# Kernel tuning notes

Hardware: AMD Instinct MI355X
Metric: run time of the kernel (lower is better)

## Reference

```python
import jax, jax.numpy as jnp
import numpy as np

B, N, K, M, CIN, O, OUT = 4, 1024, 30, 8, 9, 64, 512
BN_SCALE = 1.0 / np.sqrt(1.0 + 1e-5)  # eval-mode BatchNorm with default stats/affine


def setup_inputs() -> dict:
    key = jax.random.key(0)
    ks = jax.random.split(key, 8)
    x = jax.random.normal(ks[0], (B, CIN, N), jnp.float32)
    norm_plt = jax.random.normal(ks[1], (B, 3, N), jnp.float32)
    cls_label = jnp.zeros((B, 16), jnp.float32)
    conv1_w = jax.random.normal(ks[2], (64, 18), jnp.float32) * np.sqrt(2.0 / 18.0)
    conv1_b = jnp.zeros((64,), jnp.float32)
    sn_hw = jax.random.normal(ks[3], (4, 16, 28), jnp.float32) * np.sqrt(2.0 / 28.0)
    sn_ow = jax.random.normal(ks[4], (4, M, 16), jnp.float32) * np.sqrt(2.0 / 16.0)
    sn_ob = jnp.zeros((4, M), jnp.float32)
    mats = jax.random.normal(ks[5], (4, 2 * O, M * O), jnp.float32) * np.sqrt(2.0 / (2.0 * O))
    convt_w = jax.random.normal(ks[6], (OUT, 5 * O), jnp.float32) * np.sqrt(2.0 / (5.0 * O))
    return dict(x=x, norm_plt=norm_plt, cls_label=cls_label, conv1_w=conv1_w,
                conv1_b=conv1_b, sn_hw=sn_hw, sn_ow=sn_ow, sn_ob=sn_ob,
                mats=mats, convt_w=convt_w)


def _gather(feat, idx):
    # feat (B,N,C), idx (B,N,K) int -> (B,N,K,C): neighbor feature gather
    return jax.vmap(lambda f, i: f[i])(feat, idx)


def _bn(t):
    return t * BN_SCALE


def reference(x, norm_plt, cls_label, conv1_w, conv1_b, sn_hw, sn_ow, sn_ob, mats, convt_w):
    xt = jnp.transpose(x, (0, 2, 1))                       # (B,N,9)
    sq = jnp.sum(xt * xt, axis=-1)
    neg_d = 2.0 * jnp.einsum('bic,bjc->bij', xt, xt) - sq[:, :, None] - sq[:, None, :]
    _, idx = jax.lax.top_k(neg_d, K)                       # (B,N,K) knn indices

    nbr = _gather(xt, idx)                                 # (B,N,K,9)
    ctr = jnp.broadcast_to(xt[:, :, None, :], nbr.shape)   # (B,N,K,9)
    diff = nbr - ctr
    ed = jnp.linalg.norm(diff, axis=-1, keepdims=True)     # (B,N,K,1)
    xyz = jnp.concatenate([diff, nbr, ctr, ed], axis=-1)   # (B,N,K,28) scorenet input

    # get_graph_feature -> conv1 (1x1) -> BN -> relu -> max over k
    gf = jnp.concatenate([diff, ctr], axis=-1)             # (B,N,K,18)
    h = jax.nn.relu(_bn(jnp.einsum('bnkc,oc->bnko', gf, conv1_w) + conv1_b))
    x1 = jnp.max(h, axis=2)                                # (B,N,64)

    feats = [x1]
    f = x1
    for l in range(4):  # PAConv layers 2..5 (sequential, fixed count)
        hid = jax.nn.relu(_bn(jnp.einsum('bnkc,hc->bnkh', xyz, sn_hw[l])))
        score = jax.nn.softmax(jnp.einsum('bnkh,mh->bnkm', hid, sn_ow[l]) + sn_ob[l], axis=-1)
        kern = mats[l]                                     # (128, M*64)
        # feat_trans_dgcnn: neighbor uses full kernel on [f;f], center uses top half
        point = (jnp.concatenate([f, f], axis=-1) @ kern).reshape(B, N, M, O)
        center = (f @ kern[:O]).reshape(B, N, M, O)
        # assemble_dgcnn: sum_k sum_m score * (point[knn] - center)
        gp = _gather(point.reshape(B, N, M * O), idx).reshape(B, N, K, M, O)
        out = jnp.einsum('bnkm,bnkmo->bno', score, gp) - jnp.einsum('bnkm,bnmo->bno', score, center)
        f = jax.nn.relu(_bn(out))
        feats.append(f)

    xx = jnp.concatenate(feats, axis=-1)                   # (B,N,320)
    xc = jax.nn.relu(_bn(jnp.einsum('bnc,oc->bno', xx, convt_w)))
    return jnp.max(xc, axis=1)                             # (B,512) global max pool
```

## Files before the change

kernel.cpp:

```cpp
#include <hip/hip_runtime.h>
#include <hip/hip_bf16.h>

#define B 4
#define N 1024
#define KNN 30
#define MM 8
#define OO 64
#define OUTC 512
#define HID 16
#define FD 320
#define BNS 0.9999950000374997f

typedef float f32x4 __attribute__((ext_vector_type(4)));
typedef short s16x8 __attribute__((ext_vector_type(8)));

#define OFF_XT     0
#define OFF_SQ     36864
#define OFF_IDX    40960
#define OFF_CVT    163840
#define OFF_K2T    245760
#define OFF_FB     376832

__global__ void __launch_bounds__(256) k_prep(const float* __restrict__ x,
                                              const float* __restrict__ convt_w,
                                              const float* __restrict__ mats,
                                              float* __restrict__ xt,
                                              float* __restrict__ sq,
                                              __hip_bfloat16* __restrict__ cvt_bf,
                                              __hip_bfloat16* __restrict__ k2t_bf,
                                              float* __restrict__ out) {
  __shared__ float tile[64][65];
  if (blockIdx.x < 640) {
    int id = blockIdx.x * 256 + threadIdx.x;
    if (id < B * N) {
      int b = id >> 10, n = id & 1023;
      float s = 0.f;
#pragma unroll
      for (int c = 0; c < 9; c++) {
        float v = x[(b * 9 + c) * N + n];
        xt[id * 9 + c] = v;
        s = fmaf(v, v, s);
      }
      sq[id] = s;
    }
    if (id < B * OUTC) out[id] = 0.f;
    if (id < 512 * 320) cvt_bf[id] = __float2bfloat16(convt_w[id]);
  } else {
    int blk = blockIdx.x - 640;
    int l = blk >> 4, part = (blk >> 3) & 1, m = blk & 7;
    int tr = threadIdx.x >> 6;
    int tc = threadIdx.x & 63;
    const float* src = mats + l * 65536 + (part * 64) * 512 + m * 64;
#pragma unroll
    for (int it = 0; it < 16; it++) {
      int c = it * 4 + tr;
      tile[c][tc] = src[c * 512 + tc];
    }
    __syncthreads();
    __hip_bfloat16* dst = k2t_bf + l * 65536 + part * 512 + m * 64;
#pragma unroll
    for (int it = 0; it < 16; it++) {
      int o = it * 4 + tr;
      dst[o * 1024 + tc] = __float2bfloat16(tile[tc][o]);
    }
  }
}

__global__ void __launch_bounds__(256) k_knn(const float* __restrict__ xt,
                                             const float* __restrict__ sq,
                                             int* __restrict__ idx) {
  int r = threadIdx.x >> 6;
  int lane = threadIdx.x & 63;
  int row = blockIdx.x * 4 + r;
  int b = row >> 10;
  __shared__ unsigned int hist[4][256];
  __shared__ unsigned int cntr[4];
  __shared__ unsigned int bp[4];
  __shared__ int bn[4];
  const float* xb = xt + (b << 10) * 9;
  const float* sb = sq + (b << 10);
  float cx[9];
#pragma unroll
  for (int c = 0; c < 9; c++) cx[c] = xt[row * 9 + c];
  float sqn = sq[row];
  unsigned int key[16];
#pragma unroll
  for (int s = 0; s < 16; s++) {
    int j = s * 64 + lane;
    const float* xj = xb + j * 9;
    float dot = 0.f;
#pragma unroll
    for (int c = 0; c < 9; c++) dot = fmaf(cx[c], xj[c], dot);
    float v = 2.0f * dot - sqn - sb[j];
    unsigned int u = __float_as_uint(v);
    key[s] = u ^ ((unsigned int)(((int)u) >> 31) | 0x80000000u);
  }
  if (lane == 0) cntr[r] = 0;
  unsigned int prefix = 0;
  int need = KNN;
  for (int p = 0; p < 4; p++) {
    int shift = 24 - 8 * p;
    for (int i = lane; i < 256; i += 64) hist[r][i] = 0;
    __syncthreads();
    unsigned int himask = (p == 0) ? 0u : (0xFFFFFFFFu << (shift + 8));
#pragma unroll
    for (int s = 0; s < 16; s++) {
      if ((key[s] & himask) == prefix)
        atomicAdd(&hist[r][(key[s] >> shift) & 255], 1u);
    }
    __syncthreads();
    int c0 = hist[r][4 * lane + 0], c1 = hist[r][4 * lane + 1];
    int c2 = hist[r][4 * lane + 2], c3 = hist[r][4 * lane + 3];
    int lsum = c0 + c1 + c2 + c3;
    int sfx = lsum;
#pragma unroll
    for (int ofs = 1; ofs < 64; ofs <<= 1) {
      int t = __shfl_down(sfx, ofs, 64);
      if (lane + ofs < 64) sfx += t;
    }
    int A3 = sfx - lsum;
    int A2 = A3 + c3, A1 = A2 + c2, A0 = A1 + c1;
    if (A0 < need && need <= A0 + c0) { bp[r] = prefix | ((unsigned)(4 * lane + 0) << shift); bn[r] = need - A0; }
    if (A1 < need && need <= A1 + c1) { bp[r] = prefix | ((unsigned)(4 * lane + 1) << shift); bn[r] = need - A1; }
    if (A2 < need && need <= A2 + c2) { bp[r] = prefix | ((unsigned)(4 * lane + 2) << shift); bn[r] = need - A2; }
    if (A3 < need && need <= A3 + c3) { bp[r] = prefix | ((unsigned)(4 * lane + 3) << shift); bn[r] = need - A3; }
    __syncthreads();
    prefix = bp[r];
    need = bn[r];
  }
  unsigned int T = prefix;
  int above_total = KNN - need;
  int* orow = idx + row * KNN;
#pragma unroll
  for (int s = 0; s < 16; s++) {
    if (key[s] > T) {
      unsigned int pslot = atomicAdd(&cntr[r], 1u);
      orow[pslot] = s * 64 + lane;
    }
  }
  int base = 0;
  for (int s = 0; s < 16; s++) {
    unsigned long long m = __ballot(key[s] == T);
    if (key[s] == T) {
      int rk = base + __popcll(m & ((1ull << lane) - 1ull));
      if (rk < need) orow[above_total + rk] = s * 64 + lane;
    }
    base += __popcll(m);
    if (base >= need) break;
  }
}

__global__ void __launch_bounds__(256) k_conv1(const float* __restrict__ xt,
                                               const int* __restrict__ idx,
                                               const float* __restrict__ w,
                                               const float* __restrict__ bias,
                                               __hip_bfloat16* __restrict__ feats_bf) {
  int row0 = blockIdx.x * 4;
  int t = threadIdx.x;
  int b = row0 >> 10;
  __shared__ float ws[64 * 18];
  __shared__ __align__(16) float diff_s[4][KNN][12];
  __shared__ float ctr_s[4][9];
  for (int i = t; i < 64 * 18; i += 256) ws[i] = w[i];
  if (t < 36) { int r = t / 9, c = t - r * 9; ctr_s[r][c] = xt[(row0 + r) * 9 + c]; }
  __syncthreads();
  if (t < 120) {
    int r = t / KNN, k = t - r * KNN;
    int j = idx[(row0 + r) * KNN + k];
    const float* xj = xt + ((b << 10) + j) * 9;
#pragma unroll
    for (int c = 0; c < 9; c++) diff_s[r][k][c] = xj[c] - ctr_s[r][c];
  }
  __syncthreads();
  int wv = t >> 6, lane = t & 63;
  int row = row0 + wv;
  float wd[9];
#pragma unroll
  for (int c = 0; c < 9; c++) wd[c] = ws[lane * 18 + c];
  float cd = 0.f;
#pragma unroll
  for (int c = 0; c < 9; c++) cd = fmaf(ctr_s[wv][c], ws[lane * 18 + 9 + c], cd);
  float best = -3.0e38f;
  for (int k = 0; k < KNN; k++) {
    const float4* dr = (const float4*)diff_s[wv][k];
    float4 d0 = dr[0], d1 = dr[1], d2v = dr[2];
    float dd = 0.f;
    dd = fmaf(d0.x, wd[0], dd); dd = fmaf(d0.y, wd[1], dd);
    dd = fmaf(d0.z, wd[2], dd); dd = fmaf(d0.w, wd[3], dd);
    dd = fmaf(d1.x, wd[4], dd); dd = fmaf(d1.y, wd[5], dd);
    dd = fmaf(d1.z, wd[6], dd); dd = fmaf(d1.w, wd[7], dd);
    dd = fmaf(d2v.x, wd[8], dd);
    best = fmaxf(best, dd);
  }
  float val = (best + cd + bias[lane]) * BNS;
  feats_bf[row * FD + lane] = __float2bfloat16(fmaxf(val, 0.f));
}

__global__ void __launch_bounds__(256) k_layer(const float* __restrict__ xt,
                                               const int* __restrict__ idx,
                                               const float* __restrict__ hw,
                                               const float* __restrict__ ow,
                                               const float* __restrict__ ob,
                                               const __hip_bfloat16* __restrict__ k2t_bf,
                                               __hip_bfloat16* __restrict__ feats_bf,
                                               int l) {
  int row0 = blockIdx.x * 16;
  int t = threadIdx.x;
  int b = row0 >> 10;
  __shared__ float hws[HID * 28];
  __shared__ float ows[MM * HID];
  __shared__ float obs[MM];
  __shared__ int js[16][KNN];
  __shared__ float ctr[16][9];
  __shared__ __align__(16) float sc[16][KNN][8];
  __shared__ float ssum[16][8];
  __shared__ __align__(16) __hip_bfloat16 Hs[16][1040];
  for (int i = t; i < HID * 28; i += 256) hws[i] = hw[l * HID * 28 + i];
  if (t < MM * HID) ows[t] = ow[l * MM * HID + t];
  if (t < MM) obs[t] = ob[l * MM + t];
  if (t < 144) { int r = t / 9, c = t - r * 9; ctr[r][c] = xt[(row0 + r) * 9 + c]; }
  for (int i = t; i < 16 * KNN; i += 256) {
    int r = i / KNN, k = i - r * KNN;
    js[r][k] = (b << 10) + idx[(row0 + r) * KNN + k];
  }
  __syncthreads();
  for (int i = t; i < 16 * KNN; i += 256) {
    int r = i / KNN, k = i - r * KNN;
    const float* xj = xt + js[r][k] * 9;
    float xv[28];
    float d2 = 0.f;
#pragma unroll
    for (int c = 0; c < 9; c++) {
      float nb = xj[c], ct = ctr[r][c], df = nb - ct;
      xv[c] = df; xv[9 + c] = nb; xv[18 + c] = ct;
      d2 = fmaf(df, df, d2);
    }
    xv[27] = sqrtf(d2);
    float hid[HID];
#pragma unroll
    for (int h = 0; h < HID; h++) {
      float a = 0.f;
#pragma unroll
      for (int c = 0; c < 28; c++) a = fmaf(xv[c], hws[h * 28 + c], a);
      hid[h] = fmaxf(a * BNS, 0.f);
    }
    float lg[MM], mx = -3.0e38f;
#pragma unroll
    for (int m = 0; m < MM; m++) {
      float a = obs[m];
#pragma unroll
      for (int h = 0; h < HID; h++) a = fmaf(hid[h], ows[m * HID + h], a);
      lg[m] = a; mx = fmaxf(mx, a);
    }
    float s = 0.f;
#pragma unroll
    for (int m = 0; m < MM; m++) { lg[m] = __expf(lg[m] - mx); s += lg[m]; }
    float inv = 1.0f / s;
#pragma unroll
    for (int m = 0; m < MM; m++) sc[r][k][m] = lg[m] * inv;
  }
  __syncthreads();
  if (t < 128) {
    int r = t >> 3, m = t & 7;
    float a = 0.f;
#pragma unroll
    for (int k = 0; k < KNN; k++) a += sc[r][k][m];
    ssum[r][m] = a;
  }
  __syncthreads();
  int wv = t >> 6, lane = t & 63;
#pragma unroll
  for (int rr = 0; rr < 4; rr++) {
    int r = wv * 4 + rr;
    int row = row0 + r;
    float g[MM] = {};
#pragma unroll
    for (int k = 0; k < KNN; k++) {
      float fv = __bfloat162float(feats_bf[js[r][k] * FD + l * 64 + lane]);
      const float4* s4 = (const float4*)sc[r][k];
      float4 s0 = s4[0], s1 = s4[1];
      g[0] = fmaf(s0.x, fv, g[0]); g[1] = fmaf(s0.y, fv, g[1]);
      g[2] = fmaf(s0.z, fv, g[2]); g[3] = fmaf(s0.w, fv, g[3]);
      g[4] = fmaf(s1.x, fv, g[4]); g[5] = fmaf(s1.y, fv, g[5]);
      g[6] = fmaf(s1.z, fv, g[6]); g[7] = fmaf(s1.w, fv, g[7]);
    }
    float fn = __bfloat162float(feats_bf[row * FD + l * 64 + lane]);
#pragma unroll
    for (int m = 0; m < MM; m++) {
      Hs[r][m * 64 + lane] = __float2bfloat16(g[m] - ssum[r][m] * fn);
      Hs[r][512 + m * 64 + lane] = __float2bfloat16(g[m]);
    }
  }
  __syncthreads();
  int lr = lane & 15, lk8 = (lane >> 4) * 8;
  const short* Ks2 = (const short*)(k2t_bf + l * 65536);
  const short* brow = Ks2 + (wv * 16 + lr) * 1024 + lk8;
  const short* arow = (const short*)&Hs[lr][lk8];
  f32x4 acc = {0.f, 0.f, 0.f, 0.f};
#pragma unroll 8
  for (int kk = 0; kk < 32; kk++) {
    s16x8 a = *(const s16x8*)(arow + kk * 32);
    s16x8 bb = *(const s16x8*)(brow + kk * 32);
    acc = __builtin_amdgcn_mfma_f32_16x16x32_bf16(a, bb, acc, 0, 0, 0);
  }
#pragma unroll
  for (int i = 0; i < 4; i++) {
    int row = row0 + (lane >> 4) * 4 + i;
    feats_bf[row * FD + (l + 1) * 64 + wv * 16 + lr] =
        __float2bfloat16(fmaxf(acc[i] * BNS, 0.f));
  }
}

__global__ void __launch_bounds__(256) k_final(const __hip_bfloat16* __restrict__ feats_bf,
                                               const __hip_bfloat16* __restrict__ cvt_bf,
                                               float* __restrict__ out) {
  int m0 = (blockIdx.x >> 1) * 16;
  int nhalf = (blockIdx.x & 1) * 256;
  int w = threadIdx.x >> 6;
  int lane = threadIdx.x & 63;
  int lr = lane & 15, lk8 = (lane >> 4) * 8;
  int b = m0 >> 10;
  const short* Fs = (const short*)feats_bf;
  const short* Ws = (const short*)cvt_bf;
  const short* arow = Fs + (m0 + lr) * FD + lk8;
  int nbase = nhalf + w * 64;
  const short* brow = Ws + (nbase + lr) * FD + lk8;
  f32x4 acc[4] = {{0.f, 0.f, 0.f, 0.f}, {0.f, 0.f, 0.f, 0.f},
                  {0.f, 0.f, 0.f, 0.f}, {0.f, 0.f, 0.f, 0.f}};
#pragma unroll
  for (int kk = 0; kk < 10; kk++) {
    int k0 = kk * 32;
    s16x8 a = *(const s16x8*)(arow + k0);
#pragma unroll
    for (int tn = 0; tn < 4; tn++) {
      s16x8 bb = *(const s16x8*)(brow + tn * 16 * FD + k0);
      acc[tn] = __builtin_amdgcn_mfma_f32_16x16x32_bf16(a, bb, acc[tn], 0, 0, 0);
    }
  }
#pragma unroll
  for (int tn = 0; tn < 4; tn++) {
    float mx = fmaxf(fmaxf(acc[tn][0], acc[tn][1]), fmaxf(acc[tn][2], acc[tn][3]));
    mx = fmaxf(mx, __shfl_xor(mx, 16, 64));
    mx = fmaxf(mx, __shfl_xor(mx, 32, 64));
    if ((lane >> 4) == 0) {
      float val = fmaxf(mx * BNS, 0.f);
      int o = nbase + tn * 16 + lr;
      atomicMax((unsigned int*)out + b * OUTC + o, __float_as_uint(val));
    }
  }
}

extern "C" void kernel_launch(void* const* d_in, const int* in_sizes, int n_in,
                              void* d_out, int out_size, void* d_ws, size_t ws_size,
                              hipStream_t stream) {
  const float* x       = (const float*)d_in[0];
  const float* conv1_w = (const float*)d_in[3];
  const float* conv1_b = (const float*)d_in[4];
  const float* sn_hw   = (const float*)d_in[5];
  const float* sn_ow   = (const float*)d_in[6];
  const float* sn_ob   = (const float*)d_in[7];
  const float* mats    = (const float*)d_in[8];
  const float* convt_w = (const float*)d_in[9];
  float* out = (float*)d_out;

  float* w = (float*)d_ws;
  float* xt = w + OFF_XT;
  float* sq = w + OFF_SQ;
  int* idx = (int*)(w + OFF_IDX);
  __hip_bfloat16* cvt_bf = (__hip_bfloat16*)(w + OFF_CVT);
  __hip_bfloat16* k2t_bf = (__hip_bfloat16*)(w + OFF_K2T);
  __hip_bfloat16* feats_bf = (__hip_bfloat16*)(w + OFF_FB);

  k_prep<<<704, 256, 0, stream>>>(x, convt_w, mats, xt, sq, cvt_bf, k2t_bf, out);
  k_knn<<<1024, 256, 0, stream>>>(xt, sq, idx);
  k_conv1<<<1024, 256, 0, stream>>>(xt, idx, conv1_w, conv1_b, feats_bf);
  for (int l = 0; l < 4; l++) {
    k_layer<<<256, 256, 0, stream>>>(xt, idx, sn_hw, sn_ow, sn_ob, k2t_bf, feats_bf, l);
  }
  k_final<<<512, 256, 0, stream>>>(feats_bf, cvt_bf, out);
}
```

Measured before the change: 208.0 us.

## Fuse knn with conv1, precompute all scorenet scores, fold final conv into last layer

```diff
diff --git a/kernel.cpp b/kernel.cpp
--- a/kernel.cpp
+++ b/kernel.cpp
@@ -5,7 +5,6 @@
 #define N 1024
 #define KNN 30
 #define MM 8
-#define OO 64
 #define OUTC 512
 #define HID 16
 #define FD 320
@@ -20,6 +19,7 @@
 #define OFF_CVT    163840
 #define OFF_K2T    245760
 #define OFF_FB     376832
+#define OFF_SC     1032192
 
 __global__ void __launch_bounds__(256) k_prep(const float* __restrict__ x,
                                               const float* __restrict__ convt_w,
@@ -66,17 +66,27 @@
   }
 }
 
-__global__ void __launch_bounds__(256) k_knn(const float* __restrict__ xt,
-                                             const float* __restrict__ sq,
-                                             int* __restrict__ idx) {
-  int r = threadIdx.x >> 6;
-  int lane = threadIdx.x & 63;
+__global__ void __launch_bounds__(256) k_knnc1(const float* __restrict__ xt,
+                                               const float* __restrict__ sq,
+                                               const float* __restrict__ w,
+                                               const float* __restrict__ bias,
+                                               int* __restrict__ idx,
+                                               __hip_bfloat16* __restrict__ feats_bf) {
+  int t = threadIdx.x;
+  int r = t >> 6;
+  int lane = t & 63;
   int row = blockIdx.x * 4 + r;
   int b = row >> 10;
   __shared__ unsigned int hist[4][256];
   __shared__ unsigned int cntr[4];
   __shared__ unsigned int bp[4];
   __shared__ int bn[4];
+  __shared__ int js_l[4][KNN];
+  __shared__ float ws[64 * 18];
+  __shared__ __align__(16) float diff_s[4][KNN][12];
+  __shared__ float ctr_s[4][9];
+  for (int i = t; i < 64 * 18; i += 256) ws[i] = w[i];
+  if (t < 36) { int rr = t / 9, c = t - rr * 9; ctr_s[rr][c] = xt[(blockIdx.x * 4 + rr) * 9 + c]; }
   const float* xb = xt + (b << 10) * 9;
   const float* sb = sq + (b << 10);
   float cx[9];
@@ -115,8 +125,8 @@
     int sfx = lsum;
 #pragma unroll
     for (int ofs = 1; ofs < 64; ofs <<= 1) {
-      int t = __shfl_down(sfx, ofs, 64);
-      if (lane + ofs < 64) sfx += t;
+      int tt = __shfl_down(sfx, ofs, 64);
+      if (lane + ofs < 64) sfx += tt;
     }
     int A3 = sfx - lsum;
     int A2 = A3 + c3, A1 = A2 + c2, A0 = A1 + c1;
@@ -136,6 +146,7 @@
     if (key[s] > T) {
       unsigned int pslot = atomicAdd(&cntr[r], 1u);
       orow[pslot] = s * 64 + lane;
+      js_l[r][pslot] = s * 64 + lane;
     }
   }
   int base = 0;
@@ -143,46 +154,32 @@
     unsigned long long m = __ballot(key[s] == T);
     if (key[s] == T) {
       int rk = base + __popcll(m & ((1ull << lane) - 1ull));
-      if (rk < need) orow[above_total + rk] = s * 64 + lane;
+      if (rk < need) {
+        orow[above_total + rk] = s * 64 + lane;
+        js_l[r][above_total + rk] = s * 64 + lane;
+      }
     }
     base += __popcll(m);
     if (base >= need) break;
   }
-}
-
-__global__ void __launch_bounds__(256) k_conv1(const float* __restrict__ xt,
-                                               const int* __restrict__ idx,
-                                               const float* __restrict__ w,
-                                               const float* __restrict__ bias,
-                                               __hip_bfloat16* __restrict__ feats_bf) {
-  int row0 = blockIdx.x * 4;
-  int t = threadIdx.x;
-  int b = row0 >> 10;
-  __shared__ float ws[64 * 18];
-  __shared__ __align__(16) float diff_s[4][KNN][12];
-  __shared__ float ctr_s[4][9];
-  for (int i = t; i < 64 * 18; i += 256) ws[i] = w[i];
-  if (t < 36) { int r = t / 9, c = t - r * 9; ctr_s[r][c] = xt[(row0 + r) * 9 + c]; }
   __syncthreads();
   if (t < 120) {
-    int r = t / KNN, k = t - r * KNN;
-    int j = idx[(row0 + r) * KNN + k];
+    int rr = t / KNN, k = t - rr * KNN;
+    int j = js_l[rr][k];
     const float* xj = xt + ((b << 10) + j) * 9;
 #pragma unroll
-    for (int c = 0; c < 9; c++) diff_s[r][k][c] = xj[c] - ctr_s[r][c];
-  }
-  __syncthreads();
-  int wv = t >> 6, lane = t & 63;
-  int row = row0 + wv;
+    for (int c = 0; c < 9; c++) diff_s[rr][k][c] = xj[c] - ctr_s[rr][c];
+  }
+  __syncthreads();
   float wd[9];
 #pragma unroll
   for (int c = 0; c < 9; c++) wd[c] = ws[lane * 18 + c];
   float cd = 0.f;
 #pragma unroll
-  for (int c = 0; c < 9; c++) cd = fmaf(ctr_s[wv][c], ws[lane * 18 + 9 + c], cd);
+  for (int c = 0; c < 9; c++) cd = fmaf(ctr_s[r][c], ws[lane * 18 + 9 + c], cd);
   float best = -3.0e38f;
   for (int k = 0; k < KNN; k++) {
-    const float4* dr = (const float4*)diff_s[wv][k];
+    const float4* dr = (const float4*)diff_s[r][k];
     float4 d0 = dr[0], d1 = dr[1], d2v = dr[2];
     float dd = 0.f;
     dd = fmaf(d0.x, wd[0], dd); dd = fmaf(d0.y, wd[1], dd);
@@ -196,89 +193,99 @@
   feats_bf[row * FD + lane] = __float2bfloat16(fmaxf(val, 0.f));
 }
 
-__global__ void __launch_bounds__(256) k_layer(const float* __restrict__ xt,
+__global__ void __launch_bounds__(256) k_score(const float* __restrict__ xt,
                                                const int* __restrict__ idx,
                                                const float* __restrict__ hw,
                                                const float* __restrict__ ow,
                                                const float* __restrict__ ob,
-                                               const __hip_bfloat16* __restrict__ k2t_bf,
-                                               __hip_bfloat16* __restrict__ feats_bf,
-                                               int l) {
+                                               float* __restrict__ score) {
+  __shared__ float hws[4 * 448];
+  __shared__ float ows[4 * 128];
+  __shared__ float obs[32];
+  int t = threadIdx.x;
+  for (int i = t; i < 1792; i += 256) hws[i] = hw[i];
+  for (int i = t; i < 512; i += 256) ows[i] = ow[i];
+  if (t < 32) obs[t] = ob[t];
+  __syncthreads();
+  int id = blockIdx.x * 256 + t;
+  int row = id / KNN;
+  int b = row >> 10;
+  int j = idx[id];
+  const float* xc = xt + row * 9;
+  const float* xj = xt + ((b << 10) + j) * 9;
+  float xv[28];
+  float d2 = 0.f;
+#pragma unroll
+  for (int c = 0; c < 9; c++) {
+    float nb = xj[c], ct = xc[c], df = nb - ct;
+    xv[c] = df; xv[9 + c] = nb; xv[18 + c] = ct;
+    d2 = fmaf(df, df, d2);
+  }
+  xv[27] = sqrtf(d2);
+  for (int l = 0; l < 4; l++) {
+    float hid[HID];
+#pragma unroll
+    for (int h = 0; h < HID; h++) {
+      float a = 0.f;
+#pragma unroll
+      for (int c = 0; c < 28; c++) a = fmaf(xv[c], hws[l * 448 + h * 28 + c], a);
+      hid[h] = fmaxf(a * BNS, 0.f);
+    }
+    float lg[MM], mx = -3.0e38f;
+#pragma unroll
+    for (int m = 0; m < MM; m++) {
+      float a = obs[l * 8 + m];
+#pragma unroll
+      for (int h = 0; h < HID; h++) a = fmaf(hid[h], ows[l * 128 + m * 16 + h], a);
+      lg[m] = a; mx = fmaxf(mx, a);
+    }
+    float s = 0.f;
+#pragma unroll
+    for (int m = 0; m < MM; m++) { lg[m] = __expf(lg[m] - mx); s += lg[m]; }
+    float inv = 1.0f / s;
+    float* so = score + l * 983040 + id * 8;
+    *(float4*)so = make_float4(lg[0] * inv, lg[1] * inv, lg[2] * inv, lg[3] * inv);
+    *(float4*)(so + 4) = make_float4(lg[4] * inv, lg[5] * inv, lg[6] * inv, lg[7] * inv);
+  }
+}
+
+__global__ void __launch_bounds__(512) k_layer2(const int* __restrict__ idx,
+                                                const float* __restrict__ score,
+                                                const __hip_bfloat16* __restrict__ k2t_bf,
+                                                __hip_bfloat16* __restrict__ feats_bf,
+                                                const __hip_bfloat16* __restrict__ cvt_bf,
+                                                float* __restrict__ out,
+                                                int l, int last) {
   int row0 = blockIdx.x * 16;
   int t = threadIdx.x;
   int b = row0 >> 10;
-  __shared__ float hws[HID * 28];
-  __shared__ float ows[MM * HID];
-  __shared__ float obs[MM];
   __shared__ int js[16][KNN];
-  __shared__ float ctr[16][9];
-  __shared__ __align__(16) float sc[16][KNN][8];
   __shared__ float ssum[16][8];
   __shared__ __align__(16) __hip_bfloat16 Hs[16][1040];
-  for (int i = t; i < HID * 28; i += 256) hws[i] = hw[l * HID * 28 + i];
-  if (t < MM * HID) ows[t] = ow[l * MM * HID + t];
-  if (t < MM) obs[t] = ob[l * MM + t];
-  if (t < 144) { int r = t / 9, c = t - r * 9; ctr[r][c] = xt[(row0 + r) * 9 + c]; }
-  for (int i = t; i < 16 * KNN; i += 256) {
+  __shared__ __align__(16) __hip_bfloat16 ftile[16][336];
+  const float* sc_l = score + l * 983040;
+  for (int i = t; i < 16 * KNN; i += 512) {
     int r = i / KNN, k = i - r * KNN;
     js[r][k] = (b << 10) + idx[(row0 + r) * KNN + k];
   }
-  __syncthreads();
-  for (int i = t; i < 16 * KNN; i += 256) {
-    int r = i / KNN, k = i - r * KNN;
-    const float* xj = xt + js[r][k] * 9;
-    float xv[28];
-    float d2 = 0.f;
-#pragma unroll
-    for (int c = 0; c < 9; c++) {
-      float nb = xj[c], ct = ctr[r][c], df = nb - ct;
-      xv[c] = df; xv[9 + c] = nb; xv[18 + c] = ct;
-      d2 = fmaf(df, df, d2);
-    }
-    xv[27] = sqrtf(d2);
-    float hid[HID];
-#pragma unroll
-    for (int h = 0; h < HID; h++) {
-      float a = 0.f;
-#pragma unroll
-      for (int c = 0; c < 28; c++) a = fmaf(xv[c], hws[h * 28 + c], a);
-      hid[h] = fmaxf(a * BNS, 0.f);
-    }
-    float lg[MM], mx = -3.0e38f;
-#pragma unroll
-    for (int m = 0; m < MM; m++) {
-      float a = obs[m];
-#pragma unroll
-      for (int h = 0; h < HID; h++) a = fmaf(hid[h], ows[m * HID + h], a);
-      lg[m] = a; mx = fmaxf(mx, a);
-    }
-    float s = 0.f;
-#pragma unroll
-    for (int m = 0; m < MM; m++) { lg[m] = __expf(lg[m] - mx); s += lg[m]; }
-    float inv = 1.0f / s;
-#pragma unroll
-    for (int m = 0; m < MM; m++) sc[r][k][m] = lg[m] * inv;
-  }
-  __syncthreads();
   if (t < 128) {
     int r = t >> 3, m = t & 7;
     float a = 0.f;
-#pragma unroll
-    for (int k = 0; k < KNN; k++) a += sc[r][k][m];
+    for (int k = 0; k < KNN; k++) a += sc_l[(row0 + r) * 240 + k * 8 + m];
     ssum[r][m] = a;
   }
   __syncthreads();
   int wv = t >> 6, lane = t & 63;
 #pragma unroll
-  for (int rr = 0; rr < 4; rr++) {
-    int r = wv * 4 + rr;
+  for (int rr = 0; rr < 2; rr++) {
+    int r = wv * 2 + rr;
     int row = row0 + r;
+    const float4* srow = (const float4*)(sc_l + row * 240);
     float g[MM] = {};
 #pragma unroll
     for (int k = 0; k < KNN; k++) {
       float fv = __bfloat162float(feats_bf[js[r][k] * FD + l * 64 + lane]);
-      const float4* s4 = (const float4*)sc[r][k];
-      float4 s0 = s4[0], s1 = s4[1];
+      float4 s0 = srow[2 * k], s1 = srow[2 * k + 1];
       g[0] = fmaf(s0.x, fv, g[0]); g[1] = fmaf(s0.y, fv, g[1]);
       g[2] = fmaf(s0.z, fv, g[2]); g[3] = fmaf(s0.w, fv, g[3]);
       g[4] = fmaf(s1.x, fv, g[4]); g[5] = fmaf(s1.y, fv, g[5]);
@@ -293,59 +300,60 @@
   }
   __syncthreads();
   int lr = lane & 15, lk8 = (lane >> 4) * 8;
-  const short* Ks2 = (const short*)(k2t_bf + l * 65536);
-  const short* brow = Ks2 + (wv * 16 + lr) * 1024 + lk8;
-  const short* arow = (const short*)&Hs[lr][lk8];
-  f32x4 acc = {0.f, 0.f, 0.f, 0.f};
+  if (wv < 4) {
+    const short* Ks2 = (const short*)(k2t_bf + l * 65536);
+    const short* brow = Ks2 + (wv * 16 + lr) * 1024 + lk8;
+    const short* arow = (const short*)&Hs[lr][lk8];
+    f32x4 acc = {0.f, 0.f, 0.f, 0.f};
 #pragma unroll 8
-  for (int kk = 0; kk < 32; kk++) {
-    s16x8 a = *(const s16x8*)(arow + kk * 32);
-    s16x8 bb = *(const s16x8*)(brow + kk * 32);
-    acc = __builtin_amdgcn_mfma_f32_16x16x32_bf16(a, bb, acc, 0, 0, 0);
-  }
-#pragma unroll
-  for (int i = 0; i < 4; i++) {
-    int row = row0 + (lane >> 4) * 4 + i;
-    feats_bf[row * FD + (l + 1) * 64 + wv * 16 + lr] =
-        __float2bfloat16(fmaxf(acc[i] * BNS, 0.f));
-  }
-}
-
-__global__ void __launch_bounds__(256) k_final(const __hip_bfloat16* __restrict__ feats_bf,
-                                               const __hip_bfloat16* __restrict__ cvt_bf,
-                                               float* __restrict__ out) {
-  int m0 = (blockIdx.x >> 1) * 16;
-  int nhalf = (blockIdx.x & 1) * 256;
-  int w = threadIdx.x >> 6;
-  int lane = threadIdx.x & 63;
-  int lr = lane & 15, lk8 = (lane >> 4) * 8;
-  int b = m0 >> 10;
-  const short* Fs = (const short*)feats_bf;
-  const short* Ws = (const short*)cvt_bf;
-  const short* arow = Fs + (m0 + lr) * FD + lk8;
-  int nbase = nhalf + w * 64;
-  const short* brow = Ws + (nbase + lr) * FD + lk8;
-  f32x4 acc[4] = {{0.f, 0.f, 0.f, 0.f}, {0.f, 0.f, 0.f, 0.f},
-                  {0.f, 0.f, 0.f, 0.f}, {0.f, 0.f, 0.f, 0.f}};
-#pragma unroll
-  for (int kk = 0; kk < 10; kk++) {
-    int k0 = kk * 32;
-    s16x8 a = *(const s16x8*)(arow + k0);
+    for (int kk = 0; kk < 32; kk++) {
+      s16x8 a = *(const s16x8*)(arow + kk * 32);
+      s16x8 bb = *(const s16x8*)(brow + kk * 32);
+      acc = __builtin_amdgcn_mfma_f32_16x16x32_bf16(a, bb, acc, 0, 0, 0);
+    }
+    if (!last) {
+#pragma unroll
+      for (int i = 0; i < 4; i++) {
+        int row = row0 + (lane >> 4) * 4 + i;
+        feats_bf[row * FD + (l + 1) * 64 + wv * 16 + lr] =
+            __float2bfloat16(fmaxf(acc[i] * BNS, 0.f));
+      }
+    } else {
+#pragma unroll
+      for (int i = 0; i < 4; i++) {
+        int rl = (lane >> 4) * 4 + i;
+        ftile[rl][256 + wv * 16 + lr] = __float2bfloat16(fmaxf(acc[i] * BNS, 0.f));
+      }
+    }
+  } else if (last) {
+    int t2 = t - 256;
+    const short* Fs = (const short*)feats_bf;
+    for (int i = t2; i < 512; i += 256) {
+      int r = i >> 5, c8 = (i & 31) * 8;
+      *(s16x8*)&ftile[r][c8] = *(const s16x8*)(Fs + (row0 + r) * FD + c8);
+    }
+  }
+  if (last) {
+    __syncthreads();
+    const short* Ws = (const short*)cvt_bf;
 #pragma unroll
     for (int tn = 0; tn < 4; tn++) {
-      s16x8 bb = *(const s16x8*)(brow + tn * 16 * FD + k0);
-      acc[tn] = __builtin_amdgcn_mfma_f32_16x16x32_bf16(a, bb, acc[tn], 0, 0, 0);
-    }
-  }
-#pragma unroll
-  for (int tn = 0; tn < 4; tn++) {
-    float mx = fmaxf(fmaxf(acc[tn][0], acc[tn][1]), fmaxf(acc[tn][2], acc[tn][3]));
-    mx = fmaxf(mx, __shfl_xor(mx, 16, 64));
-    mx = fmaxf(mx, __shfl_xor(mx, 32, 64));
-    if ((lane >> 4) == 0) {
-      float val = fmaxf(mx * BNS, 0.f);
-      int o = nbase + tn * 16 + lr;
-      atomicMax((unsigned int*)out + b * OUTC + o, __float_as_uint(val));
+      int nb = wv * 64 + tn * 16;
+      const short* brow = Ws + (nb + lr) * FD + lk8;
+      f32x4 acc = {0.f, 0.f, 0.f, 0.f};
+#pragma unroll
+      for (int kk = 0; kk < 10; kk++) {
+        s16x8 a = *(const s16x8*)&ftile[lr][kk * 32 + lk8];
+        s16x8 bb = *(const s16x8*)(brow + kk * 32);
+        acc = __builtin_amdgcn_mfma_f32_16x16x32_bf16(a, bb, acc, 0, 0, 0);
+      }
+      float mx = fmaxf(fmaxf(acc[0], acc[1]), fmaxf(acc[2], acc[3]));
+      mx = fmaxf(mx, __shfl_xor(mx, 16, 64));
+      mx = fmaxf(mx, __shfl_xor(mx, 32, 64));
+      if ((lane >> 4) == 0) {
+        float val = fmaxf(mx * BNS, 0.f);
+        atomicMax((unsigned int*)out + b * OUTC + nb + lr, __float_as_uint(val));
+      }
     }
   }
 }
@@ -370,12 +378,13 @@
   __hip_bfloat16* cvt_bf = (__hip_bfloat16*)(w + OFF_CVT);
   __hip_bfloat16* k2t_bf = (__hip_bfloat16*)(w + OFF_K2T);
   __hip_bfloat16* feats_bf = (__hip_bfloat16*)(w + OFF_FB);
+  float* score = w + OFF_SC;
 
   k_prep<<<704, 256, 0, stream>>>(x, convt_w, mats, xt, sq, cvt_bf, k2t_bf, out);
-  k_knn<<<1024, 256, 0, stream>>>(xt, sq, idx);
-  k_conv1<<<1024, 256, 0, stream>>>(xt, idx, conv1_w, conv1_b, feats_bf);
+  k_knnc1<<<1024, 256, 0, stream>>>(xt, sq, conv1_w, conv1_b, idx, feats_bf);
+  k_score<<<480, 256, 0, stream>>>(xt, idx, sn_hw, sn_ow, sn_ob, score);
   for (int l = 0; l < 4; l++) {
-    k_layer<<<256, 256, 0, stream>>>(xt, idx, sn_hw, sn_ow, sn_ob, k2t_bf, feats_bf, l);
-  }
-  k_final<<<512, 256, 0, stream>>>(feats_bf, cvt_bf, out);
-}
+    k_layer2<<<256, 512, 0, stream>>>(idx, score, k2t_bf, feats_bf, cvt_bf, out,
+                                      l, l == 3 ? 1 : 0);
+  }
+}
```

Result: faster. 194.8 us (-6.4%).
